# Kernel optimization log

Hardware: AMD Instinct MI355X
Metric: run time of the kernel (lower is better)

The kernel has to match this reference:

```python
import jax, jax.numpy as jnp
import numpy as np

TEMPERATURE = 0.07
EPS = 1e-06


def setup_inputs() -> dict:
    key = jax.random.key(0)
    k1, k2 = jax.random.split(key)
    feats = jax.random.normal(k1, (8192, 512), dtype=jnp.float32)
    # module expects L2-normalized features
    feats = feats / jnp.linalg.norm(feats, axis=1, keepdims=True)
    labels = jax.random.randint(k2, (8192,), 0, 100, dtype=jnp.int64 if jax.config.jax_enable_x64 else jnp.int32)
    return {"features": feats, "labels": labels}


def reference(features, labels):
    n = features.shape[0]
    sim = jnp.matmul(features, features.T)                      # [N, N]
    lab = labels.reshape(-1, 1)
    mask = (lab == lab.T).astype(features.dtype)                # same-class mask
    logits_mask = 1.0 - jnp.eye(n, dtype=features.dtype)        # exclude self
    mask = mask * logits_mask
    logits = sim / TEMPERATURE
    logits_max = jax.lax.stop_gradient(jnp.max(logits, axis=1, keepdims=True))
    logits = logits - logits_max
    exp_logits = jnp.exp(logits) * logits_mask
    log_prob = logits - jnp.log(jnp.sum(exp_logits, axis=1, keepdims=True) + EPS)
    mean_log_prob_pos = jnp.sum(mask * log_prob, axis=1) / (jnp.sum(mask, axis=1) + EPS)
    return -jnp.mean(mean_log_prob_pos)
```

## Files before the change

kernel.cpp:

```cpp
#include <hip/hip_runtime.h>

#define NN 8192
#define KK 512
#define INVT 14.285714285714286f
#define K2E 20.60992915555662f
#define EPSF 1e-6f

#define BM 256
#define BN 64
#define CSPLIT 8
#define COLS_PER_BLOCK (NN / CSPLIT)
#define NTILES (COLS_PER_BLOCK / BN)

typedef short bf16x8 __attribute__((ext_vector_type(8)));
typedef float f32x4 __attribute__((ext_vector_type(4)));

__device__ __forceinline__ unsigned short f2bf(float f) {
  unsigned int u = __float_as_uint(f);
  u = u + 0x7FFFu + ((u >> 16) & 1u);
  return (unsigned short)(u >> 16);
}

__device__ __forceinline__ void load_lds16(const void* g, void* l) {
  __builtin_amdgcn_global_load_lds(
      (const __attribute__((address_space(1))) unsigned int*)g,
      (__attribute__((address_space(3))) unsigned int*)l, 16, 0, 0);
}

__global__ void prep_kernel(const float* __restrict__ feats,
                            const int* __restrict__ labels,
                            unsigned short* __restrict__ fb,
                            int* __restrict__ cnt) {
  int tid = blockIdx.x * 256 + threadIdx.x;
  const float4* src = (const float4*)feats + (size_t)tid * 2;
  float4 a = src[0];
  float4 b = src[1];
  bf16x8 o;
  o[0] = (short)f2bf(a.x); o[1] = (short)f2bf(a.y);
  o[2] = (short)f2bf(a.z); o[3] = (short)f2bf(a.w);
  o[4] = (short)f2bf(b.x); o[5] = (short)f2bf(b.y);
  o[6] = (short)f2bf(b.z); o[7] = (short)f2bf(b.w);
  *(bf16x8*)(fb + (size_t)tid * 8) = o;
  if (tid < NN) atomicAdd(&cnt[labels[tid]], 1);
}

__global__ __launch_bounds__(256, 1) void
scl_main_kernel(const unsigned short* __restrict__ fb,
                const int* __restrict__ labels,
                float* __restrict__ Sarr, float* __restrict__ Parr) {
  __shared__ unsigned short lds[2][BN * KK];

  const int bid = blockIdx.x;
  const int rowTile = bid / CSPLIT;
  const int colChunk = bid % CSPLIT;
  const bool diagBlk = ((rowTile >> 2) == colChunk);
  const int tid = threadIdx.x;
  const int w = tid >> 6;
  const int l = tid & 63;
  const int lo = l & 15;
  const int g = l >> 4;

  const int row0 = rowTile * BM + w * 64;
  const int colbase0 = colChunk * COLS_PER_BLOCK;

#define STAGE(buf, colbase)                                                    \
  {                                                                            \
    _Pragma("unroll") for (int j = 0; j < 16; ++j) {                           \
      const int col = w * 16 + j;                            \
      const int kc = (l & 56) | ((l ^ col) & 7);                               \
      const unsigned short* src = fb + (size_t)((colbase) + col) * KK + kc * 8;\
      load_lds16((const void*)src, (void*)&lds[buf][col * KK]);                \
    }                                                                          \
  }

  STAGE(0, colbase0);

  bf16x8 Af[4][16];
#pragma unroll
  for (int f = 0; f < 4; ++f) {
    const unsigned short* ar = fb + (size_t)(row0 + f * 16 + lo) * KK;
#pragma unroll
    for (int ks = 0; ks < 16; ++ks)
      Af[f][ks] = *(const bf16x8*)(ar + ks * 32 + g * 8);
  }

  int labr[4][4];
#pragma unroll
  for (int f = 0; f < 4; ++f)
#pragma unroll
    for (int r = 0; r < 4; ++r)
      labr[f][r] = labels[row0 + f * 16 + g * 4 + r];

  f32x4 Sac[4], Pac[4];
#pragma unroll
  for (int f = 0; f < 4; ++f) {
    Sac[f] = (f32x4){0.f, 0.f, 0.f, 0.f};
    Pac[f] = (f32x4){0.f, 0.f, 0.f, 0.f};
  }

  __syncthreads();

  for (int t = 0; t < NTILES; ++t) {
    const int cur = t & 1;
    const int colbase = colbase0 + t * BN;

    int labc[4];
#pragma unroll
    for (int st = 0; st < 4; ++st) labc[st] = labels[colbase + st * 16 + lo];

    if (t + 1 < NTILES) STAGE(cur ^ 1, colbase0 + (t + 1) * BN);

#pragma unroll
    for (int st = 0; st < 4; ++st) {
      const int ct = st * 16 + lo;
      const int colg = colbase + ct;
      f32x4 acc[4];
#pragma unroll
      for (int f = 0; f < 4; ++f) acc[f] = (f32x4){0.f, 0.f, 0.f, 0.f};
#pragma unroll
      for (int ks = 0; ks < 16; ++ks) {
        const int kc = ks * 4 + g;
        const int phys = (kc & 56) | ((kc ^ ct) & 7);
        bf16x8 Bf = *(const bf16x8*)(&lds[cur][ct * KK + phys * 8]);
#pragma unroll
        for (int f = 0; f < 4; ++f)
          acc[f] = __builtin_amdgcn_mfma_f32_16x16x32_bf16(Af[f][ks], Bf, acc[f], 0, 0, 0);
      }
#pragma unroll
      for (int f = 0; f < 4; ++f) {
#pragma unroll
        for (int r = 0; r < 4; ++r) {
          const float s = acc[f][r];
          const float e = __builtin_amdgcn_exp2f(__builtin_fmaf(s, K2E, -K2E));
          Sac[f][r] += e;
          if (labc[st] == labr[f][r]) Pac[f][r] += s;
          if (diagBlk) {
            if (colg == row0 + f * 16 + g * 4 + r) { Sac[f][r] -= e; Pac[f][r] -= s; }
          }
        }
      }
    }
    __syncthreads();
  }

#pragma unroll
  for (int f = 0; f < 4; ++f) {
#pragma unroll
    for (int r = 0; r < 4; ++r) {
      float s = Sac[f][r], p = Pac[f][r];
#pragma unroll
      for (int m = 1; m < 16; m <<= 1) {
        s += __shfl_xor(s, m, 64);
        p += __shfl_xor(p, m, 64);
      }
      if (lo == 0) {
        atomicAdd(&Sarr[row0 + f * 16 + g * 4 + r], s);
        atomicAdd(&Parr[row0 + f * 16 + g * 4 + r], p);
      }
    }
  }
#undef STAGE
}

__global__ void finish_kernel(const float* __restrict__ Sarr,
                              const float* __restrict__ Parr,
                              const int* __restrict__ labels,
                              const int* __restrict__ cnt,
                              float* __restrict__ out) {
  int i = blockIdx.x * 256 + threadIdx.x;
  float v = 0.f;
  if (i < NN) {
    float C = (float)(cnt[labels[i]] - 1);
    float lp = Parr[i] * INVT - C * (INVT + logf(Sarr[i] + EPSF));
    v = lp / (C + EPSF);
  }
#pragma unroll
  for (int m = 1; m < 64; m <<= 1) v += __shfl_xor(v, m, 64);
  if ((threadIdx.x & 63) == 0) atomicAdd(out, -v * (1.0f / NN));
}

extern "C" void kernel_launch(void* const* d_in, const int* in_sizes, int n_in,
                              void* d_out, int out_size, void* d_ws, size_t ws_size,
                              hipStream_t stream) {
  const float* feats = (const float*)d_in[0];
  const int* labels = (const int*)d_in[1];

  unsigned short* fb = (unsigned short*)d_ws;
  const size_t FB_BYTES = (size_t)NN * KK * 2;
  float* Sarr = (float*)((char*)d_ws + FB_BYTES);
  float* Parr = Sarr + NN;
  int* cnt = (int*)(Parr + NN);

  hipMemsetAsync((char*)d_ws + FB_BYTES, 0, (size_t)NN * 8 + 512, stream);
  hipMemsetAsync(d_out, 0, sizeof(float), stream);

  prep_kernel<<<dim3((NN * KK / 8) / 256), dim3(256), 0, stream>>>(feats, labels, fb, cnt);
  scl_main_kernel<<<dim3((NN / BM) * CSPLIT), dim3(256), 0, stream>>>(fb, labels, Sarr, Parr);
  finish_kernel<<<dim3(NN / 256), dim3(256), 0, stream>>>(Sarr, Parr, labels, cnt, (float*)d_out);
}
```

Measured before the change: 117.7 us.

## Restructure similarity GEMM into 256x256 output tiles with K-loop LDS pipelining

Replaces the old scheme, where each of 256 blocks held a 256-row A panel in registers and streamed its column chunk, with a conventional 256x256 output tile per block. Each block has 8 waves and loops over K in chunks of 64, double-buffering swizzled A and B tiles in LDS. It also maps blocks to XCDs so that column tiles stay local, and raises MFMA priority with setprio. Row partial sums are combined across waves in LDS before one atomic per row. The grid grows to 1024 blocks, which improves occupancy and operand reuse at the cost of more fixed overhead per tile and more LDS traffic.

```diff
diff --git a/kernel.cpp b/kernel.cpp
--- a/kernel.cpp
+++ b/kernel.cpp
@@ -7,10 +7,9 @@
 #define EPSF 1e-6f
 
 #define BM 256
-#define BN 64
-#define CSPLIT 8
-#define COLS_PER_BLOCK (NN / CSPLIT)
-#define NTILES (COLS_PER_BLOCK / BN)
+#define BN 256
+#define BK 64
+#define NKT (KK / BK)
 
 typedef short bf16x8 __attribute__((ext_vector_type(8)));
 typedef float f32x4 __attribute__((ext_vector_type(4)));
@@ -44,122 +43,147 @@
   if (tid < NN) atomicAdd(&cnt[labels[tid]], 1);
 }
 
-__global__ __launch_bounds__(256, 1) void
+__global__ __launch_bounds__(512, 2) void
 scl_main_kernel(const unsigned short* __restrict__ fb,
                 const int* __restrict__ labels,
                 float* __restrict__ Sarr, float* __restrict__ Parr) {
-  __shared__ unsigned short lds[2][BN * KK];
+  __shared__ __align__(16) unsigned short smem[65536];
 
   const int bid = blockIdx.x;
-  const int rowTile = bid / CSPLIT;
-  const int colChunk = bid % CSPLIT;
-  const bool diagBlk = ((rowTile >> 2) == colChunk);
+  const int xcd = bid & 7, q8 = bid >> 3;
+  const int colTile = xcd * 4 + (q8 >> 5);
+  const int rowTile = q8 & 31;
+  const int rowBase = rowTile * BM;
+  const int colBase = colTile * BN;
+
   const int tid = threadIdx.x;
-  const int w = tid >> 6;
-  const int l = tid & 63;
-  const int lo = l & 15;
-  const int g = l >> 4;
-
-  const int row0 = rowTile * BM + w * 64;
-  const int colbase0 = colChunk * COLS_PER_BLOCK;
-
-#define STAGE(buf, colbase)                                                    \
+  const int w = tid >> 6, l = tid & 63;
+  const int wm = w >> 2, wn = w & 3;
+  const int lo = l & 15, g = l >> 4;
+
+  const int csw = (tid & 7) ^ ((tid >> 3) & 7);
+
+#define STAGE_ONE(b, kt, i)                                                    \
   {                                                                            \
-    _Pragma("unroll") for (int j = 0; j < 16; ++j) {                           \
-      const int col = w * 16 + j;                            \
-      const int kc = (l & 56) | ((l ^ col) & 7);                               \
-      const unsigned short* src = fb + (size_t)((colbase) + col) * KK + kc * 8;\
-      load_lds16((const void*)src, (void*)&lds[buf][col * KK]);                \
-    }                                                                          \
-  }
-
-  STAGE(0, colbase0);
-
-  bf16x8 Af[4][16];
-#pragma unroll
-  for (int f = 0; f < 4; ++f) {
-    const unsigned short* ar = fb + (size_t)(row0 + f * 16 + lo) * KK;
-#pragma unroll
-    for (int ks = 0; ks < 16; ++ks)
-      Af[f][ks] = *(const bf16x8*)(ar + ks * 32 + g * 8);
-  }
-
-  int labr[4][4];
-#pragma unroll
-  for (int f = 0; f < 4; ++f)
-#pragma unroll
-    for (int r = 0; r < 4; ++r)
-      labr[f][r] = labels[row0 + f * 16 + g * 4 + r];
-
-  f32x4 Sac[4], Pac[4];
-#pragma unroll
-  for (int f = 0; f < 4; ++f) {
-    Sac[f] = (f32x4){0.f, 0.f, 0.f, 0.f};
-    Pac[f] = (f32x4){0.f, 0.f, 0.f, 0.f};
-  }
-
-  __syncthreads();
-
-  for (int t = 0; t < NTILES; ++t) {
-    const int cur = t & 1;
-    const int colbase = colbase0 + t * BN;
-
-    int labc[4];
-#pragma unroll
-    for (int st = 0; st < 4; ++st) labc[st] = labels[colbase + st * 16 + lo];
-
-    if (t + 1 < NTILES) STAGE(cur ^ 1, colbase0 + (t + 1) * BN);
-
-#pragma unroll
-    for (int st = 0; st < 4; ++st) {
-      const int ct = st * 16 + lo;
-      const int colg = colbase + ct;
-      f32x4 acc[4];
-#pragma unroll
-      for (int f = 0; f < 4; ++f) acc[f] = (f32x4){0.f, 0.f, 0.f, 0.f};
-#pragma unroll
-      for (int ks = 0; ks < 16; ++ks) {
-        const int kc = ks * 4 + g;
-        const int phys = (kc & 56) | ((kc ^ ct) & 7);
-        bf16x8 Bf = *(const bf16x8*)(&lds[cur][ct * KK + phys * 8]);
-#pragma unroll
-        for (int f = 0; f < 4; ++f)
-          acc[f] = __builtin_amdgcn_mfma_f32_16x16x32_bf16(Af[f][ks], Bf, acc[f], 0, 0, 0);
-      }
-#pragma unroll
-      for (int f = 0; f < 4; ++f) {
-#pragma unroll
-        for (int r = 0; r < 4; ++r) {
-          const float s = acc[f][r];
-          const float e = __builtin_amdgcn_exp2f(__builtin_fmaf(s, K2E, -K2E));
-          Sac[f][r] += e;
-          if (labc[st] == labr[f][r]) Pac[f][r] += s;
-          if (diagBlk) {
-            if (colg == row0 + f * 16 + g * 4 + r) { Sac[f][r] -= e; Pac[f][r] -= s; }
-          }
+    const int rl = ((i) & 3) * 64 + (tid >> 3);                                \
+    const unsigned short* src =                                                \
+        fb + (size_t)((((i) < 4) ? rowBase : colBase) + rl) * KK +             \
+        (kt) * BK + csw * 8;                                                   \
+    load_lds16((const void*)src,                                               \
+               (void*)(smem + (b) * 32768 + (((i) < 4) ? 0 : 16384) +          \
+                       ((i) & 3) * 4096 + tid * 8));                           \
+  }
+
+#pragma unroll
+  for (int i = 0; i < 8; ++i) STAGE_ONE(0, 0, i);
+
+  f32x4 acc[8][4];
+#pragma unroll
+  for (int mi = 0; mi < 8; ++mi)
+#pragma unroll
+    for (int j = 0; j < 4; ++j) acc[mi][j] = (f32x4){0.f, 0.f, 0.f, 0.f};
+
+  const int ph0 = (g ^ (lo & 7)) * 8;
+  const int ph1 = ph0 ^ 32;
+  const int aoff0 = wm * 8192 + lo * 64;
+  const int boff0 = 16384 + wn * 4096 + lo * 64;
+
+  bf16x8 Bq[4][2];
+
+#pragma unroll 2
+  for (int kt = 0; kt < NKT; ++kt) {
+    const int cur = kt & 1;
+    const int aoff = cur * 32768 + aoff0;
+    const int boff = cur * 32768 + boff0;
+    asm volatile("s_waitcnt vmcnt(0)" ::: "memory");
+    __builtin_amdgcn_s_barrier();
+
+#pragma unroll
+    for (int q = 0; q < 4; ++q) {
+      bf16x8 Aq[2][2];
+#pragma unroll
+      for (int m2 = 0; m2 < 2; ++m2) {
+        Aq[m2][0] = *(const bf16x8*)(smem + aoff + (2 * q + m2) * 1024 + ph0);
+        Aq[m2][1] = *(const bf16x8*)(smem + aoff + (2 * q + m2) * 1024 + ph1);
+      }
+      if (q == 0) {
+#pragma unroll
+        for (int j = 0; j < 4; ++j) {
+          Bq[j][0] = *(const bf16x8*)(smem + boff + j * 1024 + ph0);
+          Bq[j][1] = *(const bf16x8*)(smem + boff + j * 1024 + ph1);
         }
       }
+      if (kt + 1 < NKT) {
+        STAGE_ONE(cur ^ 1, kt + 1, 2 * q);
+        STAGE_ONE(cur ^ 1, kt + 1, 2 * q + 1);
+      }
+      __builtin_amdgcn_s_barrier();
+      asm volatile("s_waitcnt lgkmcnt(0)" ::: "memory");
+      __builtin_amdgcn_sched_barrier(0);
+      __builtin_amdgcn_s_setprio(1);
+#pragma unroll
+      for (int ks = 0; ks < 2; ++ks)
+#pragma unroll
+        for (int m2 = 0; m2 < 2; ++m2)
+#pragma unroll
+          for (int j = 0; j < 4; ++j)
+            acc[2 * q + m2][j] = __builtin_amdgcn_mfma_f32_16x16x32_bf16(
+                Aq[m2][ks], Bq[j][ks], acc[2 * q + m2][j], 0, 0, 0);
+      __builtin_amdgcn_s_setprio(0);
     }
-    __syncthreads();
-  }
-
-#pragma unroll
-  for (int f = 0; f < 4; ++f) {
+  }
+
+  int labc[4];
+#pragma unroll
+  for (int j = 0; j < 4; ++j) labc[j] = labels[colBase + wn * 64 + j * 16 + lo];
+
+  float* redS = (float*)smem;
+  float* redP = redS + 1024;
+
+#pragma unroll
+  for (int mi = 0; mi < 8; ++mi) {
+    const int rbase = rowBase + wm * 128 + mi * 16 + g * 4;
+    int labr[4];
+#pragma unroll
+    for (int r = 0; r < 4; ++r) labr[r] = labels[rbase + r];
+    f32x4 Sv = {0.f, 0.f, 0.f, 0.f}, Pv = {0.f, 0.f, 0.f, 0.f};
+#pragma unroll
+    for (int j = 0; j < 4; ++j) {
+      const int colg = colBase + wn * 64 + j * 16 + lo;
+#pragma unroll
+      for (int r = 0; r < 4; ++r) {
+        const float s = acc[mi][j][r];
+        const float e = __builtin_amdgcn_exp2f(__builtin_fmaf(s, K2E, -K2E));
+        const bool self = (colg == rbase + r);
+        if (!self) {
+          Sv[r] += e;
+          if (labc[j] == labr[r]) Pv[r] += s;
+        }
+      }
+    }
 #pragma unroll
     for (int r = 0; r < 4; ++r) {
-      float s = Sac[f][r], p = Pac[f][r];
+      float s = Sv[r], p = Pv[r];
 #pragma unroll
       for (int m = 1; m < 16; m <<= 1) {
         s += __shfl_xor(s, m, 64);
         p += __shfl_xor(p, m, 64);
       }
       if (lo == 0) {
-        atomicAdd(&Sarr[row0 + f * 16 + g * 4 + r], s);
-        atomicAdd(&Parr[row0 + f * 16 + g * 4 + r], p);
+        const int rowl = wm * 128 + mi * 16 + g * 4 + r;
+        redS[wn * 256 + rowl] = s;
+        redP[wn * 256 + rowl] = p;
       }
     }
   }
-#undef STAGE
+  __syncthreads();
+  if (tid < 256) {
+    float S = redS[tid] + redS[256 + tid] + redS[512 + tid] + redS[768 + tid];
+    float P = redP[tid] + redP[256 + tid] + redP[512 + tid] + redP[768 + tid];
+    atomicAdd(&Sarr[rowBase + tid], S);
+    atomicAdd(&Parr[rowBase + tid], P);
+  }
+#undef STAGE_ONE
 }
 
 __global__ void finish_kernel(const float* __restrict__ Sarr,
@@ -195,6 +219,6 @@
   hipMemsetAsync(d_out, 0, sizeof(float), stream);
 
   prep_kernel<<<dim3((NN * KK / 8) / 256), dim3(256), 0, stream>>>(feats, labels, fb, cnt);
-  scl_main_kernel<<<dim3((NN / BM) * CSPLIT), dim3(256), 0, stream>>>(fb, labels, Sarr, Parr);
+  scl_main_kernel<<<dim3((NN / BM) * (NN / BN)), dim3(512), 0, stream>>>(fb, labels, Sarr, Parr);
   finish_kernel<<<dim3(NN / 256), dim3(256), 0, stream>>>(Sarr, Parr, labels, cnt, (float*)d_out);
 }
```

After: 117.1 us. No clear change (-0.6%).
